# Kernel tuning notes

Measured on AMD Instinct MI355X. Metric: run time of the kernel, lower is better.

## Reference

```python
import jax, jax.numpy as jnp
import numpy as np

WINDOWS = (5, 10, 20)
EPS = 1e-4
K_SLICES = 3
OVERLAP = 0.5


def setup_inputs() -> dict:
    key = jax.random.key(0)
    k1, k2, k3, k4 = jax.random.split(key, 4)
    B, T, H = 64, 2048, 256
    x = jax.random.normal(k1, (B, T, H), dtype=jnp.float32)
    alpha = 0.1 * jax.random.normal(k2, (H, len(WINDOWS)), dtype=jnp.float32)
    gamma = 1.0 + 0.1 * jax.random.normal(k3, (K_SLICES, H), dtype=jnp.float32)
    beta = 0.1 * jax.random.normal(k4, (K_SLICES, H), dtype=jnp.float32)
    return {"x": x, "alpha": alpha, "gamma": gamma, "beta": beta}


def _fan(x, alpha):
    # FrequencyAdaptiveNormSimple: multi-window sliding mean/std, blended by softmax(alpha).
    B, T, H = x.shape
    al = jax.nn.softmax(alpha, axis=-1)  # [H, nW]
    # prefix sums for O(T) sliding statistics (same math as unfold mean/std)
    zrow = jnp.zeros((B, 1, H), x.dtype)
    S1 = jnp.concatenate([zrow, jnp.cumsum(x, axis=1)], axis=1)        # [B, T+1, H]
    S2 = jnp.concatenate([zrow, jnp.cumsum(x * x, axis=1)], axis=1)    # [B, T+1, H]
    out = jnp.zeros_like(x)
    for wi, w in enumerate(WINDOWS):
        if w > T:
            continue
        ws = S1[:, w:, :] - S1[:, : T - w + 1, :]    # window sums, [B, T-w+1, H]
        ws2 = S2[:, w:, :] - S2[:, : T - w + 1, :]
        mu = ws / w
        var = jnp.maximum((ws2 - ws * ws / w) / (w - 1), 0.0)  # unbiased (torch std default)
        sd = jnp.maximum(jnp.sqrt(var), EPS)
        # F.pad(..., (w-1, 0), mode='replicate') on the time dim
        mu = jnp.pad(mu, ((0, 0), (w - 1, 0), (0, 0)), mode="edge")
        sd = jnp.pad(sd, ((0, 0), (w - 1, 0), (0, 0)), mode="edge")
        z = jnp.nan_to_num((x - mu) / sd, nan=0.0, posinf=0.0, neginf=0.0)
        out = out + z * al[:, wi][None, None, :]
    return out


def _san(x, gamma, beta):
    # SliceAdaptiveNormSimple: overlapping slices, per-slice (B,T) stats (detached), affine, avg.
    B, T, H = x.shape
    step = max(1, int(round(T / (K_SLICES - (K_SLICES - 1) * OVERLAP))))
    win = min(T, step + int(round(step * OVERLAP)))
    y = jnp.zeros_like(x)
    cnt = jnp.zeros((B, T, 1), x.dtype)
    s = 0
    for k in range(K_SLICES):
        e = min(T, s + win)
        if e <= s:
            break
        xk = x[:, s:e, :]
        mu = jax.lax.stop_gradient(jnp.mean(xk, axis=(0, 1), keepdims=True))
        sd = jax.lax.stop_gradient(
            jnp.maximum(jnp.std(xk, axis=(0, 1), ddof=1, keepdims=True), 1e-4)
        )
        z = jnp.nan_to_num((xk - mu) / sd, nan=0.0, posinf=0.0, neginf=0.0)
        z = z * gamma[k][None, None, :] + beta[k][None, None, :]
        y = y.at[:, s:e, :].add(z)
        cnt = cnt.at[:, s:e, :].add(1.0)
        s += step
    return y / (cnt + EPS)


def reference(x, alpha, gamma, beta):
    # StableFANSAN: out = x + SAN(FAN(x))
    return x + _san(_fan(x, alpha), gamma, beta)
```

## Files before the change

kernel.cpp:

```cpp
#include <hip/hip_runtime.h>

#define T_DIM 2048
#define H_DIM 256
#define B_DIM 64
#define CHUNK 64
#define NCH (T_DIM / CHUNK)
#define NCB (B_DIM * NCH)
#define EPS_F 1e-4f

__device__ __forceinline__ void win_stats(float s1, float s2, float inv_w, float inv_wm1,
                                          float& mu, float& isd) {
    mu = s1 * inv_w;
    float var = fmaxf((s2 - s1 * s1 * inv_w) * inv_wm1, 0.0f);
    isd = fminf(rsqrtf(var), 1e4f);
}

template <int PASS, bool FIRST>
__device__ __forceinline__ void run_chunk(
    const float* __restrict__ xbh, int t0, float al0, float al1, float al2,
    float A, float Bc, float* __restrict__ outbh,
    float& ls1, float& ls2,
    float mu5i, float isd5i, float mu10i, float isd10i, float mu20i, float isd20i) {

    float s1_5 = 0.f, s2_5 = 0.f, s1_10 = 0.f, s2_10 = 0.f, s1_20 = 0.f, s2_20 = 0.f;
    float hist[32];

    if (FIRST) {
#pragma unroll
        for (int j = 0; j < 32; ++j) hist[j] = 0.0f;
    } else {
#pragma unroll
        for (int j = 1; j <= 20; ++j) {
            float v = xbh[(t0 - j) * H_DIM];
            hist[(32 - j) & 31] = v;
            s1_20 += v; s2_20 += v * v;
            if (j <= 10) { s1_10 += v; s2_10 += v * v; }
            if (j <= 5)  { s1_5  += v; s2_5  += v * v; }
        }
    }

    for (int i0 = 0; i0 < CHUNK; i0 += 32) {
#pragma unroll
        for (int k = 0; k < 32; ++k) {
            const int t = t0 + i0 + k;
            const float v = xbh[t * H_DIM];
            hist[k] = v;
            s1_5  += v; s2_5  += v * v;
            s1_10 += v; s2_10 += v * v;
            s1_20 += v; s2_20 += v * v;
            if (!FIRST || i0 + k >= 5)  { float o = hist[(k - 5)  & 31]; s1_5  -= o; s2_5  -= o * o; }
            if (!FIRST || i0 + k >= 10) { float o = hist[(k - 10) & 31]; s1_10 -= o; s2_10 -= o * o; }
            if (!FIRST || i0 + k >= 20) { float o = hist[(k - 20) & 31]; s1_20 -= o; s2_20 -= o * o; }

            float mu, isd, fan = 0.0f;
            if (!FIRST || i0 + k >= 4)  win_stats(s1_5,  s2_5,  0.2f,  0.25f,      mu, isd);
            else { mu = mu5i;  isd = isd5i; }
            fan += (v - mu) * isd * al0;
            if (!FIRST || i0 + k >= 9)  win_stats(s1_10, s2_10, 0.1f,  1.f / 9.f,  mu, isd);
            else { mu = mu10i; isd = isd10i; }
            fan += (v - mu) * isd * al1;
            if (!FIRST || i0 + k >= 19) win_stats(s1_20, s2_20, 0.05f, 1.f / 19.f, mu, isd);
            else { mu = mu20i; isd = isd20i; }
            fan += (v - mu) * isd * al2;

            if (PASS == 0) {
                ls1 += fan; ls2 += fan * fan;
            } else {
                outbh[t * H_DIM] = v + fmaf(fan, A, Bc);
            }
        }
    }
}

template <int PASS>
__global__ __launch_bounds__(256)
void fan_kernel(const float* __restrict__ x, const float* __restrict__ alpha,
                const float* __restrict__ gamma, const float* __restrict__ beta,
                float* __restrict__ part, const float* __restrict__ acc,
                float* __restrict__ out) {
    const int blk = blockIdx.x;
    const int b = blk / NCH;
    const int c = blk % NCH;
    const int h = threadIdx.x;
    const int t0 = c * CHUNK;
    const float* xbh = x + (size_t)b * T_DIM * H_DIM + h;
    float* outbh = out + (size_t)b * T_DIM * H_DIM + h;

    const float a0 = alpha[h * 3 + 0], a1 = alpha[h * 3 + 1], a2 = alpha[h * 3 + 2];
    const float mx = fmaxf(a0, fmaxf(a1, a2));
    const float e0 = __expf(a0 - mx), e1 = __expf(a1 - mx), e2 = __expf(a2 - mx);
    const float einv = 1.0f / (e0 + e1 + e2);
    const float al0 = e0 * einv, al1 = e1 * einv, al2 = e2 * einv;

    float A = 0.f, Bc = 0.f;
    if (PASS == 1) {
        const float N0 = 64.0f * 1536.0f, N1 = 64.0f * 1024.0f;
        float S10 = acc[0 * H_DIM + h], S20 = acc[1 * H_DIM + h];
        float S11 = acc[2 * H_DIM + h], S21 = acc[3 * H_DIM + h];
        float mu0 = S10 / N0;
        float v0 = fmaxf((S20 - S10 * S10 / N0) / (N0 - 1.0f), 0.0f);
        float isd0 = 1.0f / fmaxf(sqrtf(v0), EPS_F);
        float mu1 = S11 / N1;
        float v1 = fmaxf((S21 - S11 * S11 / N1) / (N1 - 1.0f), 0.0f);
        float isd1 = 1.0f / fmaxf(sqrtf(v1), EPS_F);
        float A0 = isd0 * gamma[0 * H_DIM + h], B0 = beta[0 * H_DIM + h] - mu0 * A0;
        float A1 = isd1 * gamma[1 * H_DIM + h], B1 = beta[1 * H_DIM + h] - mu1 * A1;
        const float r1 = 1.0f / 1.0001f, r2 = 1.0f / 2.0001f;
        if (c < 16)      { A = A0 * r1;        Bc = B0 * r1; }
        else if (c >= 24){ A = A1 * r1;        Bc = B1 * r1; }
        else             { A = (A0 + A1) * r2; Bc = (B0 + B1) * r2; }
    }

    float ls1 = 0.0f, ls2 = 0.0f;

    if (c == 0) {
        float mu5i, isd5i, mu10i, isd10i, mu20i, isd20i;
        float c1 = 0.f, c2 = 0.f;
#pragma unroll
        for (int j = 0; j < 20; ++j) {
            float v = xbh[j * H_DIM];
            c1 += v; c2 += v * v;
            if (j == 4)  win_stats(c1, c2, 0.2f,  0.25f,      mu5i,  isd5i);
            if (j == 9)  win_stats(c1, c2, 0.1f,  1.f / 9.f,  mu10i, isd10i);
            if (j == 19) win_stats(c1, c2, 0.05f, 1.f / 19.f, mu20i, isd20i);
        }
        run_chunk<PASS, true>(xbh, t0, al0, al1, al2, A, Bc, outbh, ls1, ls2,
                              mu5i, isd5i, mu10i, isd10i, mu20i, isd20i);
    } else {
        run_chunk<PASS, false>(xbh, t0, al0, al1, al2, A, Bc, outbh, ls1, ls2,
                               0.f, 0.f, 0.f, 0.f, 0.f, 0.f);
    }

    if (PASS == 0) {
        part[(0 * NCB + blk) * H_DIM + h] = ls1;
        part[(1 * NCB + blk) * H_DIM + h] = ls2;
    }
}

__global__ __launch_bounds__(256)
void reduce_kernel(const float* __restrict__ part, float* __restrict__ acc) {
    const int h = threadIdx.x;
    const int k = blockIdx.x >> 4;
    const int g = blockIdx.x & 15;
    float a1 = 0.f, a2 = 0.f;
    for (int i = 0; i < NCB / 16; ++i) {
        const int blk = g * (NCB / 16) + i;
        const int c = blk % NCH;
        const bool member = (k == 0) ? (c < 24) : (c >= 16);
        if (member) {
            a1 += part[(0 * NCB + blk) * H_DIM + h];
            a2 += part[(1 * NCB + blk) * H_DIM + h];
        }
    }
    atomicAdd(&acc[(2 * k)     * H_DIM + h], a1);
    atomicAdd(&acc[(2 * k + 1) * H_DIM + h], a2);
}

extern "C" void kernel_launch(void* const* d_in, const int* in_sizes, int n_in,
                              void* d_out, int out_size, void* d_ws, size_t ws_size,
                              hipStream_t stream) {
    const float* x     = (const float*)d_in[0];
    const float* alpha = (const float*)d_in[1];
    const float* gamma = (const float*)d_in[2];
    const float* beta  = (const float*)d_in[3];
    float* out  = (float*)d_out;
    float* part = (float*)d_ws;
    float* acc  = part + 2 * NCB * H_DIM;

    hipMemsetAsync(acc, 0, 4 * H_DIM * sizeof(float), stream);
    fan_kernel<0><<<NCB, H_DIM, 0, stream>>>(x, alpha, gamma, beta, part, acc, out);
    reduce_kernel<<<32, H_DIM, 0, stream>>>(part, acc);
    fan_kernel<1><<<NCB, H_DIM, 0, stream>>>(x, alpha, gamma, beta, part, acc, out);
}
```

Baseline: 365.3 us.

## Stash FAN output in fp16 and apply SAN affine in vectorized epilogue

Instead of recomputing the sliding-window FAN statistics in a second pass, the first pass writes the FAN result to a workspace stash (fp16 when the workspace is large enough, else fp32 into the output buffer). A small finalize kernel computes per-channel affine coefficients, and a float4-vectorized epilogue combines x, the stash and the coefficients. This trades recompute for extra memory traffic and introduces fp16 rounding of intermediate values.

Result: faster. 357.0 us (-2.3%).

```diff
diff --git a/kernel.cpp b/kernel.cpp
--- a/kernel.cpp
+++ b/kernel.cpp
@@ -1,4 +1,5 @@
 #include <hip/hip_runtime.h>
+#include <hip/hip_fp16.h>
 
 #define T_DIM 2048
 #define H_DIM 256
@@ -7,6 +8,8 @@
 #define NCH (T_DIM / CHUNK)
 #define NCB (B_DIM * NCH)
 #define EPS_F 1e-4f
+#define R1 (1.0f / 1.0001f)
+#define R2 (1.0f / 2.0001f)
 
 __device__ __forceinline__ void win_stats(float s1, float s2, float inv_w, float inv_wm1,
                                           float& mu, float& isd) {
@@ -15,10 +18,10 @@
     isd = fminf(rsqrtf(var), 1e4f);
 }
 
-template <int PASS, bool FIRST>
+template <int MODE, bool FIRST>
 __device__ __forceinline__ void run_chunk(
-    const float* __restrict__ xbh, int t0, float al0, float al1, float al2,
-    float A, float Bc, float* __restrict__ outbh,
+    const float* __restrict__ xbh, __half* __restrict__ s16bh, float* __restrict__ s32bh,
+    int t0, float al0, float al1, float al2,
     float& ls1, float& ls2,
     float mu5i, float isd5i, float mu10i, float isd10i, float mu20i, float isd20i) {
 
@@ -63,53 +66,33 @@
             else { mu = mu20i; isd = isd20i; }
             fan += (v - mu) * isd * al2;
 
-            if (PASS == 0) {
-                ls1 += fan; ls2 += fan * fan;
-            } else {
-                outbh[t * H_DIM] = v + fmaf(fan, A, Bc);
-            }
-        }
-    }
-}
-
-template <int PASS>
+            ls1 += fan; ls2 += fan * fan;
+            if (MODE == 0) s16bh[t * H_DIM] = __float2half(fan);
+            else           s32bh[t * H_DIM] = fan;
+        }
+    }
+}
+
+template <int MODE>
 __global__ __launch_bounds__(256)
 void fan_kernel(const float* __restrict__ x, const float* __restrict__ alpha,
-                const float* __restrict__ gamma, const float* __restrict__ beta,
-                float* __restrict__ part, const float* __restrict__ acc,
-                float* __restrict__ out) {
+                float* __restrict__ part, __half* __restrict__ stash16,
+                float* __restrict__ stash32) {
     const int blk = blockIdx.x;
     const int b = blk / NCH;
     const int c = blk % NCH;
     const int h = threadIdx.x;
     const int t0 = c * CHUNK;
-    const float* xbh = x + (size_t)b * T_DIM * H_DIM + h;
-    float* outbh = out + (size_t)b * T_DIM * H_DIM + h;
+    const size_t base = (size_t)b * T_DIM * H_DIM + h;
+    const float* xbh = x + base;
+    __half* s16bh = (MODE == 0) ? stash16 + base : nullptr;
+    float*  s32bh = (MODE == 1) ? stash32 + base : nullptr;
 
     const float a0 = alpha[h * 3 + 0], a1 = alpha[h * 3 + 1], a2 = alpha[h * 3 + 2];
     const float mx = fmaxf(a0, fmaxf(a1, a2));
     const float e0 = __expf(a0 - mx), e1 = __expf(a1 - mx), e2 = __expf(a2 - mx);
     const float einv = 1.0f / (e0 + e1 + e2);
     const float al0 = e0 * einv, al1 = e1 * einv, al2 = e2 * einv;
-
-    float A = 0.f, Bc = 0.f;
-    if (PASS == 1) {
-        const float N0 = 64.0f * 1536.0f, N1 = 64.0f * 1024.0f;
-        float S10 = acc[0 * H_DIM + h], S20 = acc[1 * H_DIM + h];
-        float S11 = acc[2 * H_DIM + h], S21 = acc[3 * H_DIM + h];
-        float mu0 = S10 / N0;
-        float v0 = fmaxf((S20 - S10 * S10 / N0) / (N0 - 1.0f), 0.0f);
-        float isd0 = 1.0f / fmaxf(sqrtf(v0), EPS_F);
-        float mu1 = S11 / N1;
-        float v1 = fmaxf((S21 - S11 * S11 / N1) / (N1 - 1.0f), 0.0f);
-        float isd1 = 1.0f / fmaxf(sqrtf(v1), EPS_F);
-        float A0 = isd0 * gamma[0 * H_DIM + h], B0 = beta[0 * H_DIM + h] - mu0 * A0;
-        float A1 = isd1 * gamma[1 * H_DIM + h], B1 = beta[1 * H_DIM + h] - mu1 * A1;
-        const float r1 = 1.0f / 1.0001f, r2 = 1.0f / 2.0001f;
-        if (c < 16)      { A = A0 * r1;        Bc = B0 * r1; }
-        else if (c >= 24){ A = A1 * r1;        Bc = B1 * r1; }
-        else             { A = (A0 + A1) * r2; Bc = (B0 + B1) * r2; }
-    }
 
     float ls1 = 0.0f, ls2 = 0.0f;
 
@@ -124,17 +107,15 @@
             if (j == 9)  win_stats(c1, c2, 0.1f,  1.f / 9.f,  mu10i, isd10i);
             if (j == 19) win_stats(c1, c2, 0.05f, 1.f / 19.f, mu20i, isd20i);
         }
-        run_chunk<PASS, true>(xbh, t0, al0, al1, al2, A, Bc, outbh, ls1, ls2,
+        run_chunk<MODE, true>(xbh, s16bh, s32bh, t0, al0, al1, al2, ls1, ls2,
                               mu5i, isd5i, mu10i, isd10i, mu20i, isd20i);
     } else {
-        run_chunk<PASS, false>(xbh, t0, al0, al1, al2, A, Bc, outbh, ls1, ls2,
+        run_chunk<MODE, false>(xbh, s16bh, s32bh, t0, al0, al1, al2, ls1, ls2,
                                0.f, 0.f, 0.f, 0.f, 0.f, 0.f);
     }
 
-    if (PASS == 0) {
-        part[(0 * NCB + blk) * H_DIM + h] = ls1;
-        part[(1 * NCB + blk) * H_DIM + h] = ls2;
-    }
+    part[(0 * NCB + blk) * H_DIM + h] = ls1;
+    part[(1 * NCB + blk) * H_DIM + h] = ls2;
 }
 
 __global__ __launch_bounds__(256)
@@ -156,6 +137,77 @@
     atomicAdd(&acc[(2 * k + 1) * H_DIM + h], a2);
 }
 
+__global__ __launch_bounds__(256)
+void finalize_kernel(const float* __restrict__ acc, const float* __restrict__ gamma,
+                     const float* __restrict__ beta, float* __restrict__ coef) {
+    const int h = threadIdx.x;
+    const float N0 = 64.0f * 1536.0f, N1 = 64.0f * 1024.0f;
+    float S10 = acc[0 * H_DIM + h], S20 = acc[1 * H_DIM + h];
+    float S11 = acc[2 * H_DIM + h], S21 = acc[3 * H_DIM + h];
+    float mu0 = S10 / N0;
+    float v0 = fmaxf((S20 - S10 * S10 / N0) / (N0 - 1.0f), 0.0f);
+    float isd0 = 1.0f / fmaxf(sqrtf(v0), EPS_F);
+    float mu1 = S11 / N1;
+    float v1 = fmaxf((S21 - S11 * S11 / N1) / (N1 - 1.0f), 0.0f);
+    float isd1 = 1.0f / fmaxf(sqrtf(v1), EPS_F);
+    float A0 = isd0 * gamma[0 * H_DIM + h];
+    float A1 = isd1 * gamma[1 * H_DIM + h];
+    coef[0 * H_DIM + h] = A0;
+    coef[1 * H_DIM + h] = beta[0 * H_DIM + h] - mu0 * A0;
+    coef[2 * H_DIM + h] = A1;
+    coef[3 * H_DIM + h] = beta[1 * H_DIM + h] - mu1 * A1;
+}
+
+template <bool HALF>
+__global__ __launch_bounds__(256)
+void epilogue_kernel(const float* __restrict__ x, const void* __restrict__ fanp,
+                     const float* __restrict__ coef, float* __restrict__ out) {
+    const int blk = blockIdx.x;
+    const int b = blk / NCH;
+    const int c = blk % NCH;
+    const int wave = threadIdx.x >> 6;
+    const int lane = threadIdx.x & 63;
+    const int h4 = lane * 4;
+
+    float4 A0 = *(const float4*)&coef[0 * H_DIM + h4];
+    float4 B0 = *(const float4*)&coef[1 * H_DIM + h4];
+    float4 A1 = *(const float4*)&coef[2 * H_DIM + h4];
+    float4 B1 = *(const float4*)&coef[3 * H_DIM + h4];
+    float4 A, Bv;
+    if (c < 16) {
+        A  = make_float4(A0.x * R1, A0.y * R1, A0.z * R1, A0.w * R1);
+        Bv = make_float4(B0.x * R1, B0.y * R1, B0.z * R1, B0.w * R1);
+    } else if (c >= 24) {
+        A  = make_float4(A1.x * R1, A1.y * R1, A1.z * R1, A1.w * R1);
+        Bv = make_float4(B1.x * R1, B1.y * R1, B1.z * R1, B1.w * R1);
+    } else {
+        A  = make_float4((A0.x + A1.x) * R2, (A0.y + A1.y) * R2, (A0.z + A1.z) * R2, (A0.w + A1.w) * R2);
+        Bv = make_float4((B0.x + B1.x) * R2, (B0.y + B1.y) * R2, (B0.z + B1.z) * R2, (B0.w + B1.w) * R2);
+    }
+
+    const int tbase = c * CHUNK + wave * 16;
+#pragma unroll 4
+    for (int i = 0; i < 16; ++i) {
+        const size_t idx = ((size_t)b * T_DIM + tbase + i) * H_DIM + h4;
+        float4 xv = *(const float4*)&x[idx];
+        float4 fv;
+        if (HALF) {
+            const __half2* fp = (const __half2*)((const __half*)fanp + idx);
+            float2 f0 = __half22float2(fp[0]);
+            float2 f1 = __half22float2(fp[1]);
+            fv = make_float4(f0.x, f0.y, f1.x, f1.y);
+        } else {
+            fv = *(const float4*)&((const float*)fanp)[idx];
+        }
+        float4 o;
+        o.x = xv.x + fmaf(fv.x, A.x, Bv.x);
+        o.y = xv.y + fmaf(fv.y, A.y, Bv.y);
+        o.z = xv.z + fmaf(fv.z, A.z, Bv.z);
+        o.w = xv.w + fmaf(fv.w, A.w, Bv.w);
+        *(float4*)&out[idx] = o;
+    }
+}
+
 extern "C" void kernel_launch(void* const* d_in, const int* in_sizes, int n_in,
                               void* d_out, int out_size, void* d_ws, size_t ws_size,
                               hipStream_t stream) {
@@ -164,11 +216,26 @@
     const float* gamma = (const float*)d_in[2];
     const float* beta  = (const float*)d_in[3];
     float* out  = (float*)d_out;
+
     float* part = (float*)d_ws;
     float* acc  = part + 2 * NCB * H_DIM;
+    float* coef = acc + 4 * H_DIM;
+    __half* stash16 = (__half*)(coef + 4 * H_DIM);
+    const size_t need = (size_t)(2 * NCB * H_DIM + 8 * H_DIM) * 4
+                      + (size_t)B_DIM * T_DIM * H_DIM * 2;
+    const bool half_path = (ws_size >= need);
 
     hipMemsetAsync(acc, 0, 4 * H_DIM * sizeof(float), stream);
-    fan_kernel<0><<<NCB, H_DIM, 0, stream>>>(x, alpha, gamma, beta, part, acc, out);
+    if (half_path) {
+        fan_kernel<0><<<NCB, H_DIM, 0, stream>>>(x, alpha, part, stash16, nullptr);
+    } else {
+        fan_kernel<1><<<NCB, H_DIM, 0, stream>>>(x, alpha, part, nullptr, out);
+    }
     reduce_kernel<<<32, H_DIM, 0, stream>>>(part, acc);
-    fan_kernel<1><<<NCB, H_DIM, 0, stream>>>(x, alpha, gamma, beta, part, acc, out);
-}
+    finalize_kernel<<<1, H_DIM, 0, stream>>>(acc, gamma, beta, coef);
+    if (half_path) {
+        epilogue_kernel<true><<<NCB, 256, 0, stream>>>(x, stash16, coef, out);
+    } else {
+        epilogue_kernel<false><<<NCB, 256, 0, stream>>>(x, out, coef, out);
+    }
+}
```
